# Kernel optimization log

Hardware: AMD Instinct MI355X
Metric: run time of the kernel (lower is better)

Reference implementation:

```python
import jax, jax.numpy as jnp
import numpy as np

N_HEAD = 16


def setup_inputs() -> dict:
    key = jax.random.key(0)
    ks = jax.random.split(key, 9)
    B, T, C = 4, 2048, 1024
    s = 1.0 / np.sqrt(C)
    x = jax.random.normal(ks[0], (B, T, C), dtype=jnp.float32)
    Wq = jax.random.normal(ks[1], (C, C), dtype=jnp.float32) * s
    bq = jnp.zeros((C,), dtype=jnp.float32)
    Wk = jax.random.normal(ks[2], (C, C), dtype=jnp.float32) * s
    bk = jnp.zeros((C,), dtype=jnp.float32)
    Wv = jax.random.normal(ks[3], (C, C), dtype=jnp.float32) * s
    bv = jnp.zeros((C,), dtype=jnp.float32)
    Wp = jax.random.normal(ks[4], (C, C), dtype=jnp.float32) * s
    bp = jnp.zeros((C,), dtype=jnp.float32)
    return {"x": x, "Wq": Wq, "bq": bq, "Wk": Wk, "bk": bk,
            "Wv": Wv, "bv": bv, "Wp": Wp, "bp": bp}


def reference(x, Wq, bq, Wk, bk, Wv, bv, Wp, bp):
    B, T, C = x.shape
    H = N_HEAD
    D = C // H
    # QKV projections, then split heads: [B, T, C] -> [B, H, T, D]
    def split_heads(t):
        return t.reshape(B, T, H, D).transpose(0, 2, 1, 3)
    q = split_heads(x @ Wq.T + bq)
    k = split_heads(x @ Wk.T + bk)
    v = split_heads(x @ Wv.T + bv)
    # NOTE: original code applies NO causal mask despite the class name.
    att = jnp.einsum('bhtd,bhsd->bhts', q, k) * (1.0 / jnp.sqrt(jnp.float32(D)))
    att = jax.nn.softmax(att, axis=-1)
    y = jnp.einsum('bhts,bhsd->bhtd', att, v)  # [B, H, T, D]
    y = y.transpose(0, 2, 1, 3).reshape(B, T, C)
    return y @ Wp.T + bp
```

## Files before the change

kernel.cpp:

```cpp
#include <hip/hip_runtime.h>
#include <hip/hip_bf16.h>

typedef float  f32x4   __attribute__((ext_vector_type(4)));
typedef short  bf16x8  __attribute__((ext_vector_type(8)));

__device__ __forceinline__ ushort f2b(float f) {
  union { float f; unsigned u; } x; x.f = f;
  unsigned r = x.u + 0x7fffu + ((x.u >> 16) & 1u);
  return (ushort)(r >> 16);
}

__device__ __forceinline__ unsigned pk2(float lo, float hi) {
  __hip_bfloat162 t = __float22bfloat162_rn(make_float2(lo, hi));
  union { __hip_bfloat162 b; unsigned u; } c; c.b = t; return c.u;
}

__device__ __forceinline__ f32x4 fzero() {
  f32x4 z; z[0] = 0.f; z[1] = 0.f; z[2] = 0.f; z[3] = 0.f; return z;
}

__device__ __forceinline__ void gld_lds16(const ushort* g, ushort* l) {
  __builtin_amdgcn_global_load_lds(g, l, 16, 0, 0);
}

__device__ __forceinline__ int vperm_s(int j64) {
  return (j64 & 0x23) | ((j64 & 0x0C) << 1) | ((j64 & 0x10) >> 2);
}

__global__ __launch_bounds__(256) void f2bf_kernel(const float* __restrict__ in,
                                                   ushort* __restrict__ out, int n4) {
  int idx = blockIdx.x * 256 + threadIdx.x;
  int stride = gridDim.x * 256;
  for (int i = idx; i < n4; i += stride) {
    float4 v = reinterpret_cast<const float4*>(in)[i];
    ushort4 o;
    o.x = f2b(v.x); o.y = f2b(v.y); o.z = f2b(v.z); o.w = f2b(v.w);
    reinterpret_cast<ushort4*>(out)[i] = o;
  }
}

__global__ __launch_bounds__(256) void f2bf_w4(
    const float* __restrict__ w0, const float* __restrict__ w1,
    const float* __restrict__ w2, const float* __restrict__ w3,
    ushort* __restrict__ out, int n4) {
  const float* src = (blockIdx.y == 0) ? w0 : (blockIdx.y == 1) ? w1
                   : (blockIdx.y == 2) ? w2 : w3;
  ushort* dst = out + (size_t)blockIdx.y * (size_t)n4 * 4;
  int idx = blockIdx.x * 256 + threadIdx.x;
  int stride = gridDim.x * 256;
  for (int i = idx; i < n4; i += stride) {
    float4 v = reinterpret_cast<const float4*>(src)[i];
    ushort4 o;
    o.x = f2b(v.x); o.y = f2b(v.y); o.z = f2b(v.z); o.w = f2b(v.w);
    reinterpret_cast<ushort4*>(dst)[i] = o;
  }
}

__global__ __launch_bounds__(256) void gemm_bt_n64(
    const ushort* __restrict__ A, const ushort* __restrict__ B,
    const float* __restrict__ bias, float* __restrict__ Cf,
    int M, int N, int K) {
  __shared__ ushort lds[18432];
  const int tid = threadIdx.x, lane = tid & 63, wave = tid >> 6;
  const int wr = (wave >> 1) << 6, wc = (wave & 1) << 5;
  const int fr = lane & 15, fk8 = (lane >> 4) << 3;

  const int orig = blockIdx.y * 16 + blockIdx.x;
  const int swz  = (orig & 7) * 128 + (orig >> 3);
  const int bx = swz & 15, by = swz >> 4;

  const size_t rowA = (size_t)by * 128;
  const size_t rowB = (size_t)bx * 64;
  const ushort* Ag = A + rowA * K;
  const ushort* Bg = B + rowB * K;

  const int c0 = tid, c1 = tid + 256;
  const size_t a0 = (size_t)(c0 >> 2) * K + (size_t)((c0 & 3) << 3);
  const size_t a1 = (size_t)(c1 >> 2) * K + (size_t)((c1 & 3) << 3);
  const ushort* sA0 = Ag + a0;
  const ushort* sA1 = Ag + a1;
  const ushort* sB0 = Bg + a0;
  const int wofs = wave * 512;

  f32x4 acc[4][2];
#pragma unroll
  for (int m = 0; m < 4; ++m)
#pragma unroll
    for (int n = 0; n < 2; ++n) acc[m][n] = fzero();

#define LD8(P) (*reinterpret_cast<const bf16x8*>(P))
#define MF16(A_, B_, C_) __builtin_amdgcn_mfma_f32_16x16x32_bf16(A_, B_, C_, 0, 0, 0)
#define STAGEP(BUF) do {                                                         \
    gld_lds16(sA0, &lds[(BUF) * 4096 + wofs]);                                   \
    gld_lds16(sA1, &lds[(BUF) * 4096 + 2048 + wofs]);                            \
    gld_lds16(sB0, &lds[12288 + (BUF) * 2048 + wofs]);                           \
    sA0 += 32; sA1 += 32; sB0 += 32;                                             \
  } while (0)
#define KSTEPP(BUF, DOPF, VMASM) do {                                            \
    if (DOPF) STAGEP(((BUF) + 2) % 3);                                           \
    bf16x8 af[4], bfv[2];                                                        \
    _Pragma("unroll")                                                            \
    for (int m = 0; m < 4; ++m)                                                  \
      af[m] = LD8(&lds[(BUF) * 4096 + (wr + m * 16 + fr) * 32 + fk8]);           \
    _Pragma("unroll")                                                            \
    for (int n = 0; n < 2; ++n)                                                  \
      bfv[n] = LD8(&lds[12288 + (BUF) * 2048 + (wc + n * 16 + fr) * 32 + fk8]);  \
    _Pragma("unroll")                                                            \
    for (int m = 0; m < 4; ++m)                                                  \
      _Pragma("unroll")                                                          \
      for (int n = 0; n < 2; ++n)                                                \
        acc[m][n] = MF16(af[m], bfv[n], acc[m][n]);                              \
    asm volatile(VMASM ::: "memory");                                            \
    __builtin_amdgcn_s_barrier();                                                \
    __builtin_amdgcn_sched_barrier(0);                                           \
  } while (0)

  STAGEP(0);
  STAGEP(1);
  asm volatile("s_waitcnt vmcnt(3)" ::: "memory");
  __builtin_amdgcn_s_barrier();
  __builtin_amdgcn_sched_barrier(0);

  for (int tb = 0; tb < 30; tb += 3) {
    KSTEPP(0, 1, "s_waitcnt vmcnt(3)");
    KSTEPP(1, 1, "s_waitcnt vmcnt(3)");
    KSTEPP(2, 1, "s_waitcnt vmcnt(3)");
  }
  KSTEPP(0, 0, "s_waitcnt vmcnt(0)");
  KSTEPP(1, 0, "");
#undef KSTEPP
#undef STAGEP
#undef MF16
#undef LD8

  const int orow = (lane >> 4) << 2;
#pragma unroll
  for (int m = 0; m < 4; ++m) {
#pragma unroll
    for (int n = 0; n < 2; ++n) {
      size_t gc = rowB + wc + n * 16 + fr;
      float bv = bias[gc];
#pragma unroll
      for (int r = 0; r < 4; ++r) {
        size_t gr = rowA + wr + m * 16 + orow + r;
        Cf[gr * N + gc] = acc[m][n][r] + bv;
      }
    }
  }
}

__global__ __launch_bounds__(256) void gemm_qkv(
    const ushort* __restrict__ A, const ushort* __restrict__ Bw,
    const float* __restrict__ bq, const float* __restrict__ bk, const float* __restrict__ bv,
    ushort* __restrict__ Qb, ushort* __restrict__ Kb, ushort* __restrict__ VbT,
    float qscale) {
  __shared__ ushort lds[24576];
  const int tid = threadIdx.x, lane = tid & 63, wave = tid >> 6;
  const int wr = (wave >> 1) << 6, wc = (wave & 1) << 6;
  const int fr = lane & 15, fk8 = (lane >> 4) << 3;
  const int K = 1024;

  const int orig = blockIdx.y * 24 + blockIdx.x;
  const int swz  = (orig & 7) * 192 + (orig >> 3);
  const int bx = swz % 24, by = swz / 24;

  const size_t rowA = (size_t)by * 128;
  const size_t rowB = (size_t)bx * 128;
  const ushort* Ag = A + rowA * K;
  const ushort* Bg = Bw + rowB * K;

  const int c0 = tid, c1 = tid + 256;
  const size_t a0 = (size_t)(c0 >> 2) * K + (size_t)((c0 & 3) << 3);
  const size_t a1 = (size_t)(c1 >> 2) * K + (size_t)((c1 & 3) << 3);
  const ushort* sA0 = Ag + a0;
  const ushort* sA1 = Ag + a1;
  const ushort* sB0 = Bg + a0;
  const ushort* sB1 = Bg + a1;
  const int wofs = wave * 512;

  f32x4 acc[4][4];
#pragma unroll
  for (int m = 0; m < 4; ++m)
#pragma unroll
    for (int n = 0; n < 4; ++n) acc[m][n] = fzero();

#define LD8(P) (*reinterpret_cast<const bf16x8*>(P))
#define MF16(A_, B_, C_) __builtin_amdgcn_mfma_f32_16x16x32_bf16(A_, B_, C_, 0, 0, 0)
#define STAGEQ(BUF) do {                                                         \
    gld_lds16(sA0, &lds[(BUF) * 4096 + wofs]);                                   \
    gld_lds16(sA1, &lds[(BUF) * 4096 + 2048 + wofs]);                            \
    gld_lds16(sB0, &lds[12288 + (BUF) * 4096 + wofs]);                           \
    gld_lds16(sB1, &lds[12288 + (BUF) * 4096 + 2048 + wofs]);                    \
    sA0 += 32; sA1 += 32; sB0 += 32; sB1 += 32;                                  \
  } while (0)
#define KSTEPQ(BUF, DOPF, VMASM) do {                                            \
    if (DOPF) STAGEQ(((BUF) + 2) % 3);                                           \
    bf16x8 af[4], bfv[4];                                                        \
    _Pragma("unroll")                                                            \
    for (int m = 0; m < 4; ++m)                                                  \
      af[m] = LD8(&lds[(BUF) * 4096 + (wr + m * 16 + fr) * 32 + fk8]);           \
    _Pragma("unroll")                                                            \
    for (int n = 0; n < 4; ++n)                                                  \
      bfv[n] = LD8(&lds[12288 + (BUF) * 4096 + (wc + n * 16 + fr) * 32 + fk8]);  \
    _Pragma("unroll")                                                            \
    for (int m = 0; m < 4; ++m)                                                  \
      _Pragma("unroll")                                                          \
      for (int n = 0; n < 4; ++n)                                                \
        acc[m][n] = MF16(af[m], bfv[n], acc[m][n]);                              \
    asm volatile(VMASM ::: "memory");                                            \
    __builtin_amdgcn_s_barrier();                                                \
    __builtin_amdgcn_sched_barrier(0);                                           \
  } while (0)

  STAGEQ(0);
  STAGEQ(1);
  asm volatile("s_waitcnt vmcnt(4)" ::: "memory");
  __builtin_amdgcn_s_barrier();
  __builtin_amdgcn_sched_barrier(0);

  for (int tb = 0; tb < 30; tb += 3) {
    KSTEPQ(0, 1, "s_waitcnt vmcnt(4)");
    KSTEPQ(1, 1, "s_waitcnt vmcnt(4)");
    KSTEPQ(2, 1, "s_waitcnt vmcnt(4)");
  }
  KSTEPQ(0, 0, "s_waitcnt vmcnt(0)");
  KSTEPQ(1, 0, "");
#undef KSTEPQ
#undef STAGEQ
#undef MF16
#undef LD8

  const int stripe  = bx >> 3;
  const int colbase = (bx & 7) * 128;
  const int orow = (lane >> 4) << 2;
#pragma unroll
  for (int m = 0; m < 4; ++m) {
#pragma unroll
    for (int n = 0; n < 4; ++n) {
      const int gcl = colbase + wc + n * 16 + fr;
      if (stripe == 0) {
        const float bb_ = bq[gcl];
#pragma unroll
        for (int r = 0; r < 4; ++r) {
          size_t gr = rowA + wr + m * 16 + orow + r;
          Qb[gr * 1024 + gcl] = f2b((acc[m][n][r] + bb_) * qscale);
        }
      } else if (stripe == 1) {
        const float bb_ = bk[gcl];
#pragma unroll
        for (int r = 0; r < 4; ++r) {
          size_t gr = rowA + wr + m * 16 + orow + r;
          Kb[gr * 1024 + gcl] = f2b(acc[m][n][r] + bb_);
        }
      } else {
        const float bb_ = bv[gcl];
        int tt0 = (int)rowA + wr + m * 16 + orow;
        int b = tt0 >> 11, t = tt0 & 2047;
        size_t idx0 = (size_t)b * 2097152 + (size_t)gcl * 2048
                    + (size_t)((t & ~63) + vperm_s(t & 63));
        ushort4 o;
        o.x = f2b(acc[m][n][0] + bb_);
        o.y = f2b(acc[m][n][1] + bb_);
        o.z = f2b(acc[m][n][2] + bb_);
        o.w = f2b(acc[m][n][3] + bb_);
        *reinterpret_cast<ushort4*>(&VbT[idx0]) = o;
      }
    }
  }
}

__global__ __launch_bounds__(512, 4) void attn_kernel(
    const ushort* __restrict__ Qb, const ushort* __restrict__ Kb,
    const ushort* __restrict__ VbT, ushort* __restrict__ Yb) {
  __shared__ ushort lds[16384];
  const int tid = threadIdx.x, lane = tid & 63, wave = tid >> 6;
  const int fr = lane & 15, g = lane >> 4, fk8 = g << 3;
  const int bb = blockIdx.y >> 4, hh = blockIdx.y & 15;
  const size_t rowbase = (size_t)bb * 2048;
  const int cbase = hh * 64;
  const ushort* Kg  = Kb  + rowbase * 1024 + cbase;
  const ushort* VgT = VbT + (size_t)bb * 2097152 + (size_t)cbase * 2048;

  const int qrow = blockIdx.x * 128 + wave * 16 + fr;
  const ushort* qptr = &Qb[(rowbase + qrow) * 1024 + cbase];
  const bf16x8 qf0 = *reinterpret_cast<const bf16x8*>(qptr + fk8);
  const bf16x8 qf1 = *reinterpret_cast<const bf16x8*>(qptr + 32 + fk8);

  const int rS = tid >> 3;
  const int wS = (tid & 7) ^ (rS & 7);
  const ushort* sKp = Kg  + (size_t)rS * 1024 + (wS << 3);
  const ushort* sVp = VgT + (size_t)rS * 2048 + (wS << 3);
  const int wofs = wave * 512;

  const int e0 = (g ^ (fr & 7)) << 3;
  const int e1 = ((4 + g) ^ (fr & 7)) << 3;
  const ushort* lpA = &lds[fr * 64 + e0];
  const ushort* lpB = &lds[fr * 64 + e1];

  f32x4 yacc[4];
#pragma unroll
  for (int nb = 0; nb < 4; ++nb) yacc[nb] = fzero();
  f32x4 psum4 = fzero();

#define LD8(P) (*reinterpret_cast<const bf16x8*>(P))
#define MF16(A, B, C) __builtin_amdgcn_mfma_f32_16x16x32_bf16(A, B, C, 0, 0, 0)

  gld_lds16(sKp, &lds[wofs]);  gld_lds16(sVp, &lds[8192 + wofs]);  sKp += 65536; sVp += 64;
  asm volatile("s_waitcnt vmcnt(0)" ::: "memory");
  __builtin_amdgcn_s_barrier();
  __builtin_amdgcn_sched_barrier(0);

#define TILE(BUF, DOPF) do {                                                     \
    if (DOPF) {    \
      gld_lds16(sKp, &lds[((BUF) ^ 1) * 4096 + wofs]);                           \
      gld_lds16(sVp, &lds[8192 + ((BUF) ^ 1) * 4096 + wofs]);                    \
      sKp += 65536; sVp += 64;                                                   \
    }                                                                            \
    f32x4 sT[4];                                                                 \
    _Pragma("unroll")                                                            \
    for (int jb = 0; jb < 4; ++jb) {                                             \
      bf16x8 kf0 = LD8(lpA + (BUF) * 4096 + jb * 1024);                          \
      bf16x8 kf1 = LD8(lpB + (BUF) * 4096 + jb * 1024);                          \
      f32x4 z = fzero();                                                         \
      __builtin_amdgcn_s_setprio(1);                                             \
      z = MF16(kf0, qf0, z);                                                     \
      z = MF16(kf1, qf1, z);                                                     \
      __builtin_amdgcn_s_setprio(0);                                             \
      sT[jb] = z;                                                                \
    }                                                                            \
    _Pragma("unroll")                                                            \
    for (int jb = 0; jb < 4; ++jb)                                               \
      _Pragma("unroll")                                                          \
      for (int r = 0; r < 4; ++r) sT[jb][r] = __builtin_exp2f(sT[jb][r]);        \
    _Pragma("unroll")                                                            \
    for (int r = 0; r < 4; ++r)                                                  \
      psum4[r] += (sT[0][r] + sT[1][r]) + (sT[2][r] + sT[3][r]);                 \
    union { bf16x8 v; unsigned u[4]; } pa0, pa1;                                 \
    pa0.u[0] = pk2(sT[0][0], sT[0][1]); pa0.u[1] = pk2(sT[0][2], sT[0][3]);      \
    pa0.u[2] = pk2(sT[1][0], sT[1][1]); pa0.u[3] = pk2(sT[1][2], sT[1][3]);      \
    pa1.u[0] = pk2(sT[2][0], sT[2][1]); pa1.u[1] = pk2(sT[2][2], sT[2][3]);      \
    pa1.u[2] = pk2(sT[3][0], sT[3][1]); pa1.u[3] = pk2(sT[3][2], sT[3][3]);      \
    _Pragma("unroll")                                                            \
    for (int nb = 0; nb < 4; ++nb) {                                             \
      bf16x8 vf0 = LD8(lpA + 8192 + (BUF) * 4096 + nb * 1024);                   \
      bf16x8 vf1 = LD8(lpB + 8192 + (BUF) * 4096 + nb * 1024);                   \
      __builtin_amdgcn_s_setprio(1);                                             \
      yacc[nb] = MF16(vf0, pa0.v, yacc[nb]);                                     \
      yacc[nb] = MF16(vf1, pa1.v, yacc[nb]);                                     \
      __builtin_amdgcn_s_setprio(0);                                             \
    }                                                                            \
    asm volatile("s_waitcnt vmcnt(0)" ::: "memory");                             \
    __builtin_amdgcn_s_barrier();                                                \
    __builtin_amdgcn_sched_barrier(0);                                           \
  } while (0)

  for (int tb = 0; tb < 30; tb += 2) {
    TILE(0, 1);
    TILE(1, 1);
  }
  TILE(0, 1);
  TILE(1, 0);
#undef TILE
#undef MF16
#undef LD8

  float psum = (psum4[0] + psum4[1]) + (psum4[2] + psum4[3]);
  psum += __shfl_xor(psum, 16);
  psum += __shfl_xor(psum, 32);
  const float linv = 1.0f / psum;
  ushort* yrow = &Yb[(rowbase + qrow) * 1024 + cbase];
#pragma unroll
  for (int nb = 0; nb < 4; ++nb) {
    ushort4 o;
    o.x = f2b(yacc[nb][0] * linv);
    o.y = f2b(yacc[nb][1] * linv);
    o.z = f2b(yacc[nb][2] * linv);
    o.w = f2b(yacc[nb][3] * linv);
    *reinterpret_cast<ushort4*>(yrow + nb * 16 + (g << 2)) = o;
  }
}

extern "C" void kernel_launch(void* const* d_in, const int* in_sizes, int n_in,
                              void* d_out, int out_size, void* d_ws, size_t ws_size,
                              hipStream_t stream) {
  const float* x  = (const float*)d_in[0];
  const float* Wq = (const float*)d_in[1];
  const float* bq = (const float*)d_in[2];
  const float* Wk = (const float*)d_in[3];
  const float* bk = (const float*)d_in[4];
  const float* Wv = (const float*)d_in[5];
  const float* bv = (const float*)d_in[6];
  const float* Wp = (const float*)d_in[7];
  const float* bp = (const float*)d_in[8];
  float* out = (float*)d_out;

  const int M = 8192, C = 1024;
  const size_t MC = (size_t)M * C, CC = (size_t)C * C;
  const size_t need = (MC * 5 + CC * 4) * sizeof(ushort);
  if (ws_size < need) return;

  ushort* xb  = (ushort*)d_ws;
  ushort* wqb = xb + MC;
  ushort* wpb = wqb + 3 * CC;
  ushort* Qb  = wpb + CC;
  ushort* Kb  = Qb + MC;
  ushort* VbT = Kb + MC;
  ushort* Yb  = VbT + MC;

  f2bf_kernel<<<2048, 256, 0, stream>>>(x, xb, (int)(MC / 4));
  f2bf_w4<<<dim3(256, 4), 256, 0, stream>>>(Wq, Wk, Wv, Wp, wqb, (int)(CC / 4));

  const float QSCALE = 0.18033688011112042f;
  gemm_qkv<<<dim3(24, 64), 256, 0, stream>>>(xb, wqb, bq, bk, bv, Qb, Kb, VbT, QSCALE);

  attn_kernel<<<dim3(16, 64), 512, 0, stream>>>(Qb, Kb, VbT, Yb);

  gemm_bt_n64<<<dim3(16, 64), 256, 0, stream>>>(Yb, wpb, bp, out, M, C, C);
}
```

Baseline: 225.6 us.

## Software-pipeline attention tiles so QK of next tile overlaps softmax-PV of previous

Restructures the attention inner loop so that each iteration computes QK^T scores for the current KV tile while applying exp, packing and the PV MFMAs to the previous tile's scores. V fragments are preloaded into registers, and the loop gains an explicit prologue and epilogue. The intent is to hide exp and transcendental latency behind independent MFMA work. Launch bounds are relaxed from 4 to 2 blocks per CU to make room for the extra live registers, which risks lower occupancy.

Measured after the change: 243.3 us. 1.08x slower.

```diff
diff --git a/kernel.cpp b/kernel.cpp
--- a/kernel.cpp
+++ b/kernel.cpp
@@ -269,7 +269,7 @@
   }
 }
 
-__global__ __launch_bounds__(512, 4) void attn_kernel(
+__global__ __launch_bounds__(512, 2) void attn_kernel(
     const ushort* __restrict__ Qb, const ushort* __restrict__ Kb,
     const ushort* __restrict__ VbT, ushort* __restrict__ Yb) {
   __shared__ ushort lds[16384];
@@ -301,66 +301,94 @@
 #pragma unroll
   for (int nb = 0; nb < 4; ++nb) yacc[nb] = fzero();
   f32x4 psum4 = fzero();
+  f32x4 sTo[4];
+  bf16x8 vfo[8];
 
 #define LD8(P) (*reinterpret_cast<const bf16x8*>(P))
 #define MF16(A, B, C) __builtin_amdgcn_mfma_f32_16x16x32_bf16(A, B, C, 0, 0, 0)
-
-  gld_lds16(sKp, &lds[wofs]);  gld_lds16(sVp, &lds[8192 + wofs]);  sKp += 65536; sVp += 64;
-  asm volatile("s_waitcnt vmcnt(0)" ::: "memory");
-  __builtin_amdgcn_s_barrier();
-  __builtin_amdgcn_sched_barrier(0);
-
-#define TILE(BUF, DOPF) do {                                                     \
-    if (DOPF) {    \
-      gld_lds16(sKp, &lds[((BUF) ^ 1) * 4096 + wofs]);                           \
-      gld_lds16(sVp, &lds[8192 + ((BUF) ^ 1) * 4096 + wofs]);                    \
-      sKp += 65536; sVp += 64;                                                   \
-    }                                                                            \
-    f32x4 sT[4];                                                                 \
+#define STAGE(BUF) do {                                                          \
+    gld_lds16(sKp, &lds[(BUF) * 4096 + wofs]);                                   \
+    gld_lds16(sVp, &lds[8192 + (BUF) * 4096 + wofs]);                            \
+    sKp += 65536; sVp += 64;                                                     \
+  } while (0)
+#define QKBLK(BUF, DST) do {                                                     \
     _Pragma("unroll")                                                            \
     for (int jb = 0; jb < 4; ++jb) {                                             \
       bf16x8 kf0 = LD8(lpA + (BUF) * 4096 + jb * 1024);                          \
       bf16x8 kf1 = LD8(lpB + (BUF) * 4096 + jb * 1024);                          \
       f32x4 z = fzero();                                                         \
-      __builtin_amdgcn_s_setprio(1);                                             \
       z = MF16(kf0, qf0, z);                                                     \
       z = MF16(kf1, qf1, z);                                                     \
-      __builtin_amdgcn_s_setprio(0);                                             \
-      sT[jb] = z;                                                                \
+      DST[jb] = z;                                                               \
     }                                                                            \
+  } while (0)
+#define VLOAD(BUF) do {                                                          \
+    _Pragma("unroll")                                                            \
+    for (int nb = 0; nb < 4; ++nb) {                                             \
+      vfo[2 * nb]     = LD8(lpA + 8192 + (BUF) * 4096 + nb * 1024);              \
+      vfo[2 * nb + 1] = LD8(lpB + 8192 + (BUF) * 4096 + nb * 1024);              \
+    }                                                                            \
+  } while (0)
+#define SMPV() do {                                                              \
     _Pragma("unroll")                                                            \
     for (int jb = 0; jb < 4; ++jb)                                               \
       _Pragma("unroll")                                                          \
-      for (int r = 0; r < 4; ++r) sT[jb][r] = __builtin_exp2f(sT[jb][r]);        \
+      for (int r = 0; r < 4; ++r) sTo[jb][r] = __builtin_exp2f(sTo[jb][r]);      \
     _Pragma("unroll")                                                            \
     for (int r = 0; r < 4; ++r)                                                  \
-      psum4[r] += (sT[0][r] + sT[1][r]) + (sT[2][r] + sT[3][r]);                 \
+      psum4[r] += (sTo[0][r] + sTo[1][r]) + (sTo[2][r] + sTo[3][r]);             \
     union { bf16x8 v; unsigned u[4]; } pa0, pa1;                                 \
-    pa0.u[0] = pk2(sT[0][0], sT[0][1]); pa0.u[1] = pk2(sT[0][2], sT[0][3]);      \
-    pa0.u[2] = pk2(sT[1][0], sT[1][1]); pa0.u[3] = pk2(sT[1][2], sT[1][3]);      \
-    pa1.u[0] = pk2(sT[2][0], sT[2][1]); pa1.u[1] = pk2(sT[2][2], sT[2][3]);      \
-    pa1.u[2] = pk2(sT[3][0], sT[3][1]); pa1.u[3] = pk2(sT[3][2], sT[3][3]);      \
+    pa0.u[0] = pk2(sTo[0][0], sTo[0][1]); pa0.u[1] = pk2(sTo[0][2], sTo[0][3]);  \
+    pa0.u[2] = pk2(sTo[1][0], sTo[1][1]); pa0.u[3] = pk2(sTo[1][2], sTo[1][3]);  \
+    pa1.u[0] = pk2(sTo[2][0], sTo[2][1]); pa1.u[1] = pk2(sTo[2][2], sTo[2][3]);  \
+    pa1.u[2] = pk2(sTo[3][0], sTo[3][1]); pa1.u[3] = pk2(sTo[3][2], sTo[3][3]);  \
+    __builtin_amdgcn_s_setprio(1);                                               \
     _Pragma("unroll")                                                            \
     for (int nb = 0; nb < 4; ++nb) {                                             \
-      bf16x8 vf0 = LD8(lpA + 8192 + (BUF) * 4096 + nb * 1024);                   \
-      bf16x8 vf1 = LD8(lpB + 8192 + (BUF) * 4096 + nb * 1024);                   \
-      __builtin_amdgcn_s_setprio(1);                                             \
-      yacc[nb] = MF16(vf0, pa0.v, yacc[nb]);                                     \
-      yacc[nb] = MF16(vf1, pa1.v, yacc[nb]);                                     \
-      __builtin_amdgcn_s_setprio(0);                                             \
+      yacc[nb] = MF16(vfo[2 * nb],     pa0.v, yacc[nb]);                         \
+      yacc[nb] = MF16(vfo[2 * nb + 1], pa1.v, yacc[nb]);                         \
     }                                                                            \
+    __builtin_amdgcn_s_setprio(0);                                               \
+  } while (0)
+#define TILE(BUF, DOPF) do {                                                     \
+    if (DOPF) STAGE((BUF) ^ 1);                                                  \
+    f32x4 sTn[4];                                                                \
+    QKBLK(BUF, sTn);                                                             \
+    SMPV();                   \
+    VLOAD(BUF);                                  \
+    _Pragma("unroll")                                                            \
+    for (int jb = 0; jb < 4; ++jb) sTo[jb] = sTn[jb];                            \
+    asm volatile("s_waitcnt lgkmcnt(0)" ::: "memory");                           \
     asm volatile("s_waitcnt vmcnt(0)" ::: "memory");                             \
     __builtin_amdgcn_s_barrier();                                                \
     __builtin_amdgcn_sched_barrier(0);                                           \
   } while (0)
 
-  for (int tb = 0; tb < 30; tb += 2) {
+  STAGE(0);
+  asm volatile("s_waitcnt vmcnt(0)" ::: "memory");
+  __builtin_amdgcn_s_barrier();
+  __builtin_amdgcn_sched_barrier(0);
+
+  STAGE(1);
+  QKBLK(0, sTo);
+  VLOAD(0);
+  asm volatile("s_waitcnt lgkmcnt(0)" ::: "memory");
+  asm volatile("s_waitcnt vmcnt(0)" ::: "memory");
+  __builtin_amdgcn_s_barrier();
+  __builtin_amdgcn_sched_barrier(0);
+
+  for (int tb = 1; tb < 31; tb += 2) {
+    TILE(1, 1);
     TILE(0, 1);
-    TILE(1, 1);
-  }
-  TILE(0, 1);
+  }
   TILE(1, 0);
+
+  SMPV();
 #undef TILE
+#undef SMPV
+#undef VLOAD
+#undef QKBLK
+#undef STAGE
 #undef MF16
 #undef LD8
 
```
